# Optimization experiments

Hardware: AMD Instinct MI355X
Metric: run time of the kernel (lower is better)

The kernel has to match this reference:

```python
import jax, jax.numpy as jnp
import numpy as np

D = 256      # d_model
H = 8        # n_heads
L = 6        # n_layers
F = 1024     # ffn_hidden
MAXB = 50    # max_boids
S = MAXB + 3 # seq len: CLS + ctx + predator + boids
B = 4096
VH = 256     # value_hidden_dim
DH = D // H


def setup_inputs() -> dict:
    key = jax.random.key(0)
    ks = jax.random.split(key, 20)
    r = lambda i, shape: jax.random.normal(ks[i], shape, jnp.float32) * 0.02
    return {
        "observation": jax.random.normal(ks[0], (B, 4 + 4 * MAXB), jnp.float32),
        "cls_emb": r(1, (D,)), "type_cls": r(2, (D,)), "type_ctx": r(3, (D,)),
        "type_pred": r(4, (D,)), "type_boid": r(5, (D,)),
        "ctx_W": r(6, (2, D)), "ctx_b": jnp.zeros((D,), jnp.float32),
        "pred_W": r(7, (4, D)), "pred_b": jnp.zeros((D,), jnp.float32),
        "boid_W": r(8, (4, D)), "boid_b": jnp.zeros((D,), jnp.float32),
        "qkv_W": r(9, (L, D, 3 * D)), "qkv_b": jnp.zeros((L, 3 * D), jnp.float32),
        "out_W": r(10, (L, D, D)), "out_b": jnp.zeros((L, D), jnp.float32),
        "ln1_g": jnp.ones((L, D), jnp.float32), "ln1_b": jnp.zeros((L, D), jnp.float32),
        "ffn_W1": r(11, (L, D, F)), "ffn_b1": jnp.zeros((L, F), jnp.float32),
        "ffn_W2": r(12, (L, F, D)), "ffn_b2": jnp.zeros((L, D), jnp.float32),
        "ln2_g": jnp.ones((L, D), jnp.float32), "ln2_b": jnp.zeros((L, D), jnp.float32),
        "proj_W": r(13, (D, 2)), "proj_b": jnp.zeros((2,), jnp.float32),
        "vh_W1": r(14, (D, VH)), "vh_b1": jnp.zeros((VH,), jnp.float32),
        "vh_W2": r(15, (VH, VH)), "vh_b2": jnp.zeros((VH,), jnp.float32),
        "vh_W3": r(16, (VH, 1)), "vh_b3": jnp.zeros((1,), jnp.float32),
    }


def _ln(x, g, b):
    m = jnp.mean(x, axis=-1, keepdims=True)
    v = jnp.mean((x - m) ** 2, axis=-1, keepdims=True)
    return (x - m) * jax.lax.rsqrt(v + 1e-5) * g + b


def reference(observation, cls_emb, type_cls, type_ctx, type_pred, type_boid,
              ctx_W, ctx_b, pred_W, pred_b, boid_W, boid_b,
              qkv_W, qkv_b, out_W, out_b, ln1_g, ln1_b,
              ffn_W1, ffn_b1, ffn_W2, ffn_b2, ln2_g, ln2_b,
              proj_W, proj_b, vh_W1, vh_b1, vh_W2, vh_b2, vh_W3, vh_b3):
    Bn = observation.shape[0]
    ctx = observation[:, :2]                                   # [B,2]
    pred = jnp.concatenate([observation[:, 2:4],
                            jnp.zeros_like(observation[:, :2])], axis=-1)  # [B,4]
    boids = observation[:, 4:].reshape(Bn, MAXB, 4)            # [B,MAXB,4]

    # All-zero boid slots are skipped; valid boids are packed to the front
    # (stable order preserved), then zero-padded -- vectorized via stable argsort.
    valid = jnp.any(boids != 0, axis=-1)                       # [B,MAXB]
    order = jnp.argsort(~valid, axis=1, stable=True)           # valid first
    packed = jnp.take_along_axis(boids, order[:, :, None], axis=1)
    vs = jnp.take_along_axis(valid, order, axis=1)             # [B,MAXB]

    cls_tok = jnp.broadcast_to(cls_emb + type_cls, (Bn, 1, D))
    ctx_tok = (ctx @ ctx_W + ctx_b + type_ctx)[:, None, :]
    pred_tok = (pred @ pred_W + pred_b + type_pred)[:, None, :]
    boid_tok = (packed @ boid_W + boid_b + type_boid) * vs[:, :, None]  # pad -> zeros
    x = jnp.concatenate([cls_tok, ctx_tok, pred_tok, boid_tok], axis=1)  # [B,S,D]

    pad = jnp.concatenate([jnp.zeros((Bn, 3), bool), ~vs], axis=1)       # [B,S]
    neg = jnp.where(pad, -1e9, 0.0)[:, None, None, :]                    # [B,1,1,S]

    scale = 1.0 / np.sqrt(DH)
    for i in range(L):  # post-LN encoder layers (ReLU FFN)
        qkv = x @ qkv_W[i] + qkv_b[i]                                    # [B,S,3D]
        q, k, v = jnp.split(qkv, 3, axis=-1)
        q = q.reshape(Bn, S, H, DH).transpose(0, 2, 1, 3)
        k = k.reshape(Bn, S, H, DH).transpose(0, 2, 1, 3)
        v = v.reshape(Bn, S, H, DH).transpose(0, 2, 1, 3)
        scores = jnp.einsum('bhqd,bhkd->bhqk', q, k) * scale + neg
        a = jax.nn.softmax(scores, axis=-1)
        o = jnp.einsum('bhqk,bhkd->bhqd', a, v).transpose(0, 2, 1, 3).reshape(Bn, S, D)
        x = _ln(x + o @ out_W[i] + out_b[i], ln1_g[i], ln1_b[i])
        h = jax.nn.relu(x @ ffn_W1[i] + ffn_b1[i])
        x = _ln(x + h @ ffn_W2[i] + ffn_b2[i], ln2_g[i], ln2_b[i])

    cls_f = x[:, 0]                                                      # [B,D]
    action_mean = jnp.tanh(cls_f @ proj_W + proj_b)                      # [B,2]
    h = jax.nn.relu(cls_f @ vh_W1 + vh_b1)
    h = jax.nn.relu(h @ vh_W2 + vh_b2)
    value = h @ vh_W3 + vh_b3                                            # [B,1]
    return jnp.concatenate([action_mean, value], axis=-1)                # [B,3]
```

## Files before the change

### kernel.cpp

```cpp
#include <hip/hip_runtime.h>
#include <hip/hip_bf16.h>
#include <stdint.h>

typedef unsigned short u16;
typedef short s16x8 __attribute__((ext_vector_type(8)));
typedef float f32x4 __attribute__((ext_vector_type(4)));

#define D_ 256
#define H_ 8
#define L_ 6
#define F_ 1024
#define MAXB_ 50
#define S_ 53
#define B_ 4096

__device__ __forceinline__ u16 f2b(float f){
  __hip_bfloat16 h = __float2bfloat16(f);
  return *reinterpret_cast<u16*>(&h);
}
__device__ __forceinline__ float b2f(u16 u){
  __hip_bfloat16 h = *reinterpret_cast<__hip_bfloat16*>(&u);
  return __bfloat162float(h);
}

__device__ __forceinline__ void gload16(const void* g, void* l){
  __builtin_amdgcn_global_load_lds((__attribute__((address_space(1))) void*)(g),
                                   (__attribute__((address_space(3))) void*)(l), 16, 0, 0);
}

__global__ __launch_bounds__(256) void prep_weights(
    const float* __restrict__ qkvW, const float* __restrict__ outW,
    const float* __restrict__ w1,   const float* __restrict__ w2,
    u16* __restrict__ qkvT, u16* __restrict__ outT,
    u16* __restrict__ w1T,  u16* __restrict__ w2T)
{
  const int i = blockIdx.x * 256 + threadIdx.x;
  if (i < L_*768*256) {
    const int l = i / (768*256); const int r = i % (768*256);
    const int n = r >> 8; const int k = r & 255;
    qkvT[i] = f2b(qkvW[((size_t)l*256 + k)*768 + n]);
  }
  if (i < L_*256*256) {
    const int l = i >> 16; const int r = i & 65535;
    const int n = r >> 8; const int k = r & 255;
    outT[i] = f2b(outW[((size_t)l*256 + k)*256 + n]);
  }
  if (i < L_*1024*256) {
    const int l = i / (1024*256); const int r = i % (1024*256);
    const int n = r >> 8; const int k = r & 255;
    w1T[i] = f2b(w1[((size_t)l*256 + k)*1024 + n]);
  }
  if (i < L_*256*1024) {
    const int l = i / (256*1024); const int r = i % (256*1024);
    const int n = r >> 10; const int k = r & 1023;
    w2T[i] = f2b(w2[((size_t)l*1024 + k)*256 + n]);
  }
}

__global__ __launch_bounds__(256) void embed_kernel(
    const float* __restrict__ obs,
    const float* __restrict__ cls_emb, const float* __restrict__ type_cls,
    const float* __restrict__ type_ctx, const float* __restrict__ type_pred,
    const float* __restrict__ type_boid,
    const float* __restrict__ ctxW, const float* __restrict__ ctxb,
    const float* __restrict__ predW, const float* __restrict__ predb,
    const float* __restrict__ boidW, const float* __restrict__ boidb,
    u16* __restrict__ xbf, int* __restrict__ nvalid)
{
  const int b = blockIdx.x, tid = threadIdx.x;
  __shared__ float obs_s[204];
  __shared__ int perm_s[MAXB_];
  __shared__ int count_s;
  const float* orow = obs + (size_t)b * 204;
  if (tid < 204) obs_s[tid] = orow[tid];
  __syncthreads();
  if (tid < 64) {
    const int j = tid;
    bool flag = false;
    if (j < MAXB_) {
      const float a0=obs_s[4+4*j], a1=obs_s[5+4*j], a2=obs_s[6+4*j], a3=obs_s[7+4*j];
      flag = (a0!=0.f)||(a1!=0.f)||(a2!=0.f)||(a3!=0.f);
    }
    const unsigned long long m = __ballot(flag);
    if (flag) perm_s[__popcll(m & ((1ull<<j)-1ull))] = j;
    if (j == 0) { count_s = __popcll(m); nvalid[b] = __popcll(m); }
  }
  __syncthreads();
  const int cnt = count_s;
  const int d = tid;
  for (int s = 0; s < S_; ++s) {
    float v;
    if (s == 0)      v = cls_emb[d] + type_cls[d];
    else if (s == 1) v = obs_s[0]*ctxW[d] + obs_s[1]*ctxW[256+d] + ctxb[d] + type_ctx[d];
    else if (s == 2) v = obs_s[2]*predW[d] + obs_s[3]*predW[256+d] + predb[d] + type_pred[d];
    else {
      const int j = s - 3;
      if (j < cnt) {
        const int bj = perm_s[j];
        v = obs_s[4+4*bj]*boidW[d] + obs_s[5+4*bj]*boidW[256+d]
          + obs_s[6+4*bj]*boidW[512+d] + obs_s[7+4*bj]*boidW[768+d]
          + boidb[d] + type_boid[d];
      } else v = 0.f;
    }
    xbf[((size_t)b*S_ + s)*256 + d] = f2b(v);
  }
}

template<bool RELU>
__global__ __launch_bounds__(256, 2) void gemm_bias_kernel(
    const u16* __restrict__ A, const u16* __restrict__ Bt,
    const float* __restrict__ bias, u16* __restrict__ C,
    int N, int K)
{
  __shared__ __attribute__((aligned(16))) u16 As[128*64];
  __shared__ __attribute__((aligned(16))) u16 Bs[128*64];
  const int tid = threadIdx.x;
  const int w = tid >> 6, lane = tid & 63;
  const int wr = w >> 1, wc = w & 1;
  const int lm = lane & 15, lg = lane >> 4;
  const int lrow = lane >> 3, lcol = (lane & 7) * 8;
  const int m0 = blockIdx.x * 128, n0 = blockIdx.y * 128;

  f32x4 acc[4][4];
  #pragma unroll
  for (int m=0;m<4;m++)
    #pragma unroll
    for (int n=0;n<4;n++)
      #pragma unroll
      for (int t=0;t<4;t++) acc[m][n][t] = 0.f;

  for (int k0 = 0; k0 < K; k0 += 64) {
    #pragma unroll
    for (int j=0;j<4;j++){
      const int chunk = w*4 + j;
      const int row = chunk*8 + lrow;
      gload16(A  + (size_t)(m0+row)*K + k0 + lcol, &As[chunk*512]);
      gload16(Bt + (size_t)(n0+row)*K + k0 + lcol, &Bs[chunk*512]);
    }
    __syncthreads();
    #pragma unroll
    for (int kk=0;kk<64;kk+=32){
      s16x8 af[4], bfr[4];
      #pragma unroll
      for (int m=0;m<4;m++) af[m] = *reinterpret_cast<const s16x8*>(&As[(wr*64 + m*16 + lm)*64 + kk + lg*8]);
      #pragma unroll
      for (int n=0;n<4;n++) bfr[n] = *reinterpret_cast<const s16x8*>(&Bs[(wc*64 + n*16 + lm)*64 + kk + lg*8]);
      #pragma unroll
      for (int m=0;m<4;m++)
        #pragma unroll
        for (int n=0;n<4;n++)
          acc[m][n] = __builtin_amdgcn_mfma_f32_16x16x32_bf16(af[m], bfr[n], acc[m][n], 0, 0, 0);
    }
    __syncthreads();
  }

  #pragma unroll
  for (int n=0;n<4;n++){
    const int col = n0 + wc*64 + n*16 + lm;
    const float bv = bias[col];
    #pragma unroll
    for (int m=0;m<4;m++){
      const int r0 = m0 + wr*64 + m*16 + lg*4;
      #pragma unroll
      for (int j=0;j<4;j++){
        float v = acc[m][n][j] + bv;
        if (RELU) v = fmaxf(v, 0.f);
        C[(size_t)(r0+j)*N + col] = f2b(v);
      }
    }
  }
}

__global__ __launch_bounds__(64) void attn_kernel(
    const u16* __restrict__ qkv, u16* __restrict__ O, const int* __restrict__ nvalid)
{
  const int bh = blockIdx.x;
  const int b = bh >> 3, h = bh & 7;
  const int lane = threadIdx.x;
  const int lm = lane & 15, lg = lane >> 4;
  __shared__ __attribute__((aligned(16))) u16 Pl[64*72];
  __shared__ __attribute__((aligned(16))) u16 VT[32*72];
  const size_t base = (size_t)b * S_ * 768;

  s16x8 aQ[4], aK[4];
  #pragma unroll
  for (int t=0;t<4;t++){
    const int r = t*16 + lm;
    if (r < S_){
      aQ[t] = *reinterpret_cast<const s16x8*>(&qkv[base + (size_t)r*768 +       h*32 + lg*8]);
      aK[t] = *reinterpret_cast<const s16x8*>(&qkv[base + (size_t)r*768 + 256 + h*32 + lg*8]);
    } else {
      #pragma unroll
      for (int i=0;i<8;i++){ aQ[t][i]=0; aK[t][i]=0; }
    }
  }
  {
    const int s = lane;
    #pragma unroll
    for (int i4=0;i4<4;i4++){
      s16x8 v;
      if (s < S_) v = *reinterpret_cast<const s16x8*>(&qkv[base + (size_t)s*768 + 512 + h*32 + i4*8]);
      else {
        #pragma unroll
        for (int i=0;i<8;i++) v[i]=0;
      }
      #pragma unroll
      for (int t=0;t<8;t++) VT[(i4*8+t)*72 + s] = (u16)v[t];
    }
  }
  f32x4 zf;
  #pragma unroll
  for (int t=0;t<4;t++) zf[t] = 0.f;
  f32x4 sc[4][4];
  #pragma unroll
  for (int qi=0;qi<4;qi++)
    #pragma unroll
    for (int kj=0;kj<4;kj++)
      sc[qi][kj] = __builtin_amdgcn_mfma_f32_16x16x32_bf16(aQ[qi], aK[kj], zf, 0, 0, 0);

  const int T = 3 + nvalid[b];
  const float scale = 0.17677669529663689f;
  __syncthreads();

  #pragma unroll
  for (int qi=0;qi<4;qi++){
    #pragma unroll
    for (int j=0;j<4;j++){
      float v[4];
      #pragma unroll
      for (int kj=0;kj<4;kj++)
        v[kj] = sc[qi][kj][j]*scale + ((kj*16+lm) < T ? 0.f : -1e9f);
      float mx = fmaxf(fmaxf(v[0],v[1]), fmaxf(v[2],v[3]));
      mx = fmaxf(mx, __shfl_xor(mx, 1));
      mx = fmaxf(mx, __shfl_xor(mx, 2));
      mx = fmaxf(mx, __shfl_xor(mx, 4));
      mx = fmaxf(mx, __shfl_xor(mx, 8));
      float e[4]; float sum = 0.f;
      #pragma unroll
      for (int kj=0;kj<4;kj++){ e[kj] = __expf(v[kj]-mx); sum += e[kj]; }
      sum += __shfl_xor(sum, 1);
      sum += __shfl_xor(sum, 2);
      sum += __shfl_xor(sum, 4);
      sum += __shfl_xor(sum, 8);
      const float inv = 1.f / sum;
      const int q = qi*16 + lg*4 + j;
      #pragma unroll
      for (int kj=0;kj<4;kj++) Pl[q*72 + kj*16 + lm] = f2b(e[kj]*inv);
    }
  }
  __syncthreads();

  s16x8 bV[2][2];
  #pragma unroll
  for (int c=0;c<2;c++)
    #pragma unroll
    for (int dj=0;dj<2;dj++)
      bV[c][dj] = *reinterpret_cast<const s16x8*>(&VT[(dj*16+lm)*72 + c*32 + lg*8]);

  f32x4 oa[4][2];
  #pragma unroll
  for (int qi=0;qi<4;qi++)
    #pragma unroll
    for (int dj=0;dj<2;dj++)
      #pragma unroll
      for (int t=0;t<4;t++) oa[qi][dj][t] = 0.f;

  #pragma unroll
  for (int qi=0;qi<4;qi++){
    #pragma unroll
    for (int c=0;c<2;c++){
      const s16x8 aP = *reinterpret_cast<const s16x8*>(&Pl[(qi*16+lm)*72 + c*32 + lg*8]);
      #pragma unroll
      for (int dj=0;dj<2;dj++)
        oa[qi][dj] = __builtin_amdgcn_mfma_f32_16x16x32_bf16(aP, bV[c][dj], oa[qi][dj], 0, 0, 0);
    }
  }
  #pragma unroll
  for (int qi=0;qi<4;qi++)
    #pragma unroll
    for (int dj=0;dj<2;dj++)
      #pragma unroll
      for (int j=0;j<4;j++){
        const int q = qi*16 + lg*4 + j;
        if (q < S_)
          O[((size_t)(b*S_ + q))*256 + h*32 + dj*16 + lm] = f2b(oa[qi][dj][j]);
      }
}

__global__ __launch_bounds__(256, 2) void gemm_ln_kernel(
    const u16* __restrict__ A, const u16* __restrict__ Bt,
    const float* __restrict__ bias, const float* __restrict__ lng, const float* __restrict__ lnb,
    u16* __restrict__ xbf, int K)
{
  __shared__ __attribute__((aligned(16))) u16 As[64*64];
  __shared__ __attribute__((aligned(16))) u16 Bs[256*64];
  __shared__ float redS[4][64];
  __shared__ float redQ[4][64];
  const int tid = threadIdx.x;
  const int w = tid >> 6, lane = tid & 63;
  const int lm = lane & 15, lg = lane >> 4;
  const int lrow = lane >> 3, lcol = (lane & 7)*8;
  const int m0 = blockIdx.x * 64;

  f32x4 acc[4][4];
  #pragma unroll
  for (int m=0;m<4;m++)
    #pragma unroll
    for (int n=0;n<4;n++)
      #pragma unroll
      for (int t=0;t<4;t++) acc[m][n][t] = 0.f;

  for (int k0 = 0; k0 < K; k0 += 64) {
    #pragma unroll
    for (int j=0;j<2;j++){
      const int chunk = w*2 + j;
      const int row = chunk*8 + lrow;
      gload16(A + (size_t)(m0+row)*K + k0 + lcol, &As[chunk*512]);
    }
    #pragma unroll
    for (int j=0;j<8;j++){
      const int chunk = w*8 + j;
      const int row = chunk*8 + lrow;
      gload16(Bt + (size_t)row*K + k0 + lcol, &Bs[chunk*512]);
    }
    __syncthreads();
    #pragma unroll
    for (int kk=0;kk<64;kk+=32){
      s16x8 af[4], bfr[4];
      #pragma unroll
      for (int m=0;m<4;m++) af[m] = *reinterpret_cast<const s16x8*>(&As[(m*16 + lm)*64 + kk + lg*8]);
      #pragma unroll
      for (int n=0;n<4;n++) bfr[n] = *reinterpret_cast<const s16x8*>(&Bs[(w*64 + n*16 + lm)*64 + kk + lg*8]);
      #pragma unroll
      for (int m=0;m<4;m++)
        #pragma unroll
        for (int n=0;n<4;n++)
          acc[m][n] = __builtin_amdgcn_mfma_f32_16x16x32_bf16(af[m], bfr[n], acc[m][n], 0, 0, 0);
    }
    __syncthreads();
  }

  float bb[4];
  #pragma unroll
  for (int n=0;n<4;n++) bb[n] = bias[w*64 + n*16 + lm];
  #pragma unroll
  for (int m=0;m<4;m++)
    #pragma unroll
    for (int j=0;j<4;j++){
      const int r = m*16 + lg*4 + j;
      const u16* resp = xbf + (size_t)(m0+r)*256 + w*64 + lm;
      #pragma unroll
      for (int n=0;n<4;n++) acc[m][n][j] += bb[n] + b2f(resp[n*16]);
    }

  #pragma unroll
  for (int m=0;m<4;m++)
    #pragma unroll
    for (int j=0;j<4;j++){
      float s1 = 0.f, s2 = 0.f;
      #pragma unroll
      for (int n=0;n<4;n++){ const float t = acc[m][n][j]; s1 += t; s2 += t*t; }
      s1 += __shfl_xor(s1, 1); s2 += __shfl_xor(s2, 1);
      s1 += __shfl_xor(s1, 2); s2 += __shfl_xor(s2, 2);
      s1 += __shfl_xor(s1, 4); s2 += __shfl_xor(s2, 4);
      s1 += __shfl_xor(s1, 8); s2 += __shfl_xor(s2, 8);
      if (lm == 0){ const int r = m*16 + lg*4 + j; redS[w][r] = s1; redQ[w][r] = s2; }
    }
  __syncthreads();

  float gg[4], be[4];
  #pragma unroll
  for (int n=0;n<4;n++){ const int col = w*64 + n*16 + lm; gg[n] = lng[col]; be[n] = lnb[col]; }
  #pragma unroll
  for (int m=0;m<4;m++)
    #pragma unroll
    for (int j=0;j<4;j++){
      const int r = m*16 + lg*4 + j;
      const float sum = redS[0][r]+redS[1][r]+redS[2][r]+redS[3][r];
      const float sq  = redQ[0][r]+redQ[1][r]+redQ[2][r]+redQ[3][r];
      const float mean = sum * (1.f/256.f);
      const float var  = sq  * (1.f/256.f) - mean*mean;
      const float rstd = rsqrtf(var + 1e-5f);
      #pragma unroll
      for (int n=0;n<4;n++){
        const float y = (acc[m][n][j] - mean)*rstd*gg[n] + be[n];
        xbf[(size_t)(m0+r)*256 + w*64 + n*16 + lm] = f2b(y);
      }
    }
}

__global__ __launch_bounds__(256) void head_kernel(
    const u16* __restrict__ xbf,
    const float* __restrict__ projW, const float* __restrict__ projb,
    const float* __restrict__ W1, const float* __restrict__ b1,
    const float* __restrict__ W2, const float* __restrict__ b2,
    const float* __restrict__ W3, const float* __restrict__ b3,
    float* __restrict__ out)
{
  const int b = blockIdx.x, tid = threadIdx.x;
  __shared__ float c_s[256];
  __shared__ float h_s[256];
  __shared__ float red[3][4];
  const float c = b2f(xbf[((size_t)b*S_)*256 + tid]);
  c_s[tid] = c;
  __syncthreads();
  float a1 = b1[tid];
  #pragma unroll 8
  for (int k=0;k<256;k++) a1 += c_s[k]*W1[k*256+tid];
  a1 = fmaxf(a1, 0.f);
  h_s[tid] = a1;
  __syncthreads();
  float a2 = b2[tid];
  #pragma unroll 8
  for (int k=0;k<256;k++) a2 += h_s[k]*W2[k*256+tid];
  a2 = fmaxf(a2, 0.f);

  float pv = a2 * W3[tid];
  float p0 = c * projW[tid*2];
  float p1 = c * projW[tid*2+1];
  #pragma unroll
  for (int o=1;o<64;o<<=1){
    pv += __shfl_xor(pv, o);
    p0 += __shfl_xor(p0, o);
    p1 += __shfl_xor(p1, o);
  }
  const int w = tid >> 6;
  if ((tid & 63) == 0){ red[0][w]=p0; red[1][w]=p1; red[2][w]=pv; }
  __syncthreads();
  if (tid == 0){
    const float q0 = red[0][0]+red[0][1]+red[0][2]+red[0][3] + projb[0];
    const float q1 = red[1][0]+red[1][1]+red[1][2]+red[1][3] + projb[1];
    const float qv = red[2][0]+red[2][1]+red[2][2]+red[2][3] + b3[0];
    out[b*3+0] = tanhf(q0);
    out[b*3+1] = tanhf(q1);
    out[b*3+2] = qv;
  }
}

__global__ void fallback_ws(float* out, int n, float val){
  const int i = blockIdx.x*256 + threadIdx.x;
  if (i < n) out[i] = val;
}

extern "C" void kernel_launch(void* const* d_in, const int* in_sizes, int n_in,
                              void* d_out, int out_size, void* d_ws, size_t ws_size,
                              hipStream_t stream)
{
  (void)in_sizes; (void)n_in;
  const float* obs      = (const float*)d_in[0];
  const float* cls_emb  = (const float*)d_in[1];
  const float* type_cls = (const float*)d_in[2];
  const float* type_ctx = (const float*)d_in[3];
  const float* type_pred= (const float*)d_in[4];
  const float* type_boid= (const float*)d_in[5];
  const float* ctx_W    = (const float*)d_in[6];
  const float* ctx_b    = (const float*)d_in[7];
  const float* pred_W   = (const float*)d_in[8];
  const float* pred_b   = (const float*)d_in[9];
  const float* boid_W   = (const float*)d_in[10];
  const float* boid_b   = (const float*)d_in[11];
  const float* qkv_W    = (const float*)d_in[12];
  const float* qkv_b    = (const float*)d_in[13];
  const float* out_W    = (const float*)d_in[14];
  const float* out_b    = (const float*)d_in[15];
  const float* ln1_g    = (const float*)d_in[16];
  const float* ln1_b    = (const float*)d_in[17];
  const float* ffn_W1   = (const float*)d_in[18];
  const float* ffn_b1   = (const float*)d_in[19];
  const float* ffn_W2   = (const float*)d_in[20];
  const float* ffn_b2   = (const float*)d_in[21];
  const float* ln2_g    = (const float*)d_in[22];
  const float* ln2_b    = (const float*)d_in[23];
  const float* proj_W   = (const float*)d_in[24];
  const float* proj_b   = (const float*)d_in[25];
  const float* vh_W1    = (const float*)d_in[26];
  const float* vh_b1    = (const float*)d_in[27];
  const float* vh_W2    = (const float*)d_in[28];
  const float* vh_b2    = (const float*)d_in[29];
  const float* vh_W3    = (const float*)d_in[30];
  const float* vh_b3    = (const float*)d_in[31];

  const size_t SZ_WQ = (size_t)L_*768*256*2;
  const size_t SZ_WO = (size_t)L_*256*256*2;
  const size_t SZ_W1 = (size_t)L_*1024*256*2;
  const size_t SZ_W2 = (size_t)L_*256*1024*2;
  const size_t SZ_W  = SZ_WQ + SZ_WO + SZ_W1 + SZ_W2;

  int Bc = 0;
  const int cand[6] = {4096, 2048, 1024, 512, 256, 128};
  for (int i = 0; i < 6; ++i) {
    const size_t need = SZ_W + (size_t)cand[i]*162816ull + (size_t)cand[i]*4ull + 4096ull;
    if (need <= ws_size) { Bc = cand[i]; break; }
  }
  if (Bc == 0) {
    const float val = 2000.0f + (float)(ws_size >> 20);
    fallback_ws<<<(out_size+255)/256, 256, 0, stream>>>((float*)d_out, out_size, val);
    return;
  }
  const int NC = B_ / Bc;
  const size_t Mc = (size_t)Bc * S_;

  char* ws = (char*)d_ws;
  u16* wq  = (u16*)(ws);
  u16* wo  = (u16*)(ws + SZ_WQ);
  u16* w1t = (u16*)(ws + SZ_WQ + SZ_WO);
  u16* w2t = (u16*)(ws + SZ_WQ + SZ_WO + SZ_W1);
  char* act = ws + SZ_W;
  u16* xbf  = (u16*)(act);
  u16* big  = (u16*)(act + Mc*512);
  u16* obuf = (u16*)(act + Mc*512 + Mc*2048);
  int* nval = (int*)(act + Mc*512 + Mc*2048 + Mc*512);

  prep_weights<<<6144, 256, 0, stream>>>(qkv_W, out_W, ffn_W1, ffn_W2, wq, wo, w1t, w2t);

  for (int c = 0; c < NC; ++c) {
    const size_t b0 = (size_t)c * Bc;
    embed_kernel<<<Bc, 256, 0, stream>>>(obs + b0*204,
        cls_emb, type_cls, type_ctx, type_pred, type_boid,
        ctx_W, ctx_b, pred_W, pred_b, boid_W, boid_b,
        xbf, nval);
    for (int l = 0; l < L_; ++l) {
      gemm_bias_kernel<false><<<dim3((int)(Mc/128), 6), 256, 0, stream>>>(
          xbf, wq + (size_t)l*768*256, qkv_b + l*768, big, 768, 256);
      attn_kernel<<<Bc*H_, 64, 0, stream>>>(big, obuf, nval);
      gemm_ln_kernel<<<(int)(Mc/64), 256, 0, stream>>>(
          obuf, wo + (size_t)l*256*256, out_b + l*256, ln1_g + l*256, ln1_b + l*256,
          xbf, 256);
      gemm_bias_kernel<true><<<dim3((int)(Mc/128), 8), 256, 0, stream>>>(
          xbf, w1t + (size_t)l*1024*256, ffn_b1 + l*1024, big, 1024, 256);
      gemm_ln_kernel<<<(int)(Mc/64), 256, 0, stream>>>(
          big, w2t + (size_t)l*256*1024, ffn_b2 + l*256, ln2_g + l*256, ln2_b + l*256,
          xbf, 1024);
    }
    head_kernel<<<Bc, 256, 0, stream>>>(xbf, proj_W, proj_b, vh_W1, vh_b1, vh_W2, vh_b2,
                                        vh_W3, vh_b3, (float*)d_out + b0*3);
  }
}
```

Before: 5.792 ms.

## Replace tiled GEMM with weight-stationary register GEMM, swizzle LDS in LN GEMM

The QKV and FFN1 GEMMs become a weight-stationary persistent kernel. Each wave keeps a 32-column slice of the weight matrix in registers for the full K=256 and loops over 16-row strips of A read straight from global memory, with no LDS staging. The gemm_ln kernel gets an XOR swizzle on its LDS layout to cut bank conflicts. The batch chunk size is now derived from the available workspace in multiples of 64 instead of powers of two, so more of the batch fits in one chunk. The risks are that A is re-read from global without LDS reuse and that the weight slice raises register pressure.

```diff
diff --git a/kernel.cpp b/kernel.cpp
--- a/kernel.cpp
+++ b/kernel.cpp
@@ -106,68 +106,50 @@
   }
 }
 
-template<bool RELU>
-__global__ __launch_bounds__(256, 2) void gemm_bias_kernel(
+template<int N, bool RELU>
+__global__ __launch_bounds__(256, 3) void wsgemm_kernel(
     const u16* __restrict__ A, const u16* __restrict__ Bt,
-    const float* __restrict__ bias, u16* __restrict__ C,
-    int N, int K)
-{
-  __shared__ __attribute__((aligned(16))) u16 As[128*64];
-  __shared__ __attribute__((aligned(16))) u16 Bs[128*64];
+    const float* __restrict__ bias, u16* __restrict__ C, int M)
+{
   const int tid = threadIdx.x;
   const int w = tid >> 6, lane = tid & 63;
-  const int wr = w >> 1, wc = w & 1;
   const int lm = lane & 15, lg = lane >> 4;
-  const int lrow = lane >> 3, lcol = (lane & 7) * 8;
-  const int m0 = blockIdx.x * 128, n0 = blockIdx.y * 128;
-
-  f32x4 acc[4][4];
-  #pragma unroll
-  for (int m=0;m<4;m++)
-    #pragma unroll
-    for (int n=0;n<4;n++)
-      #pragma unroll
-      for (int t=0;t<4;t++) acc[m][n][t] = 0.f;
-
-  for (int k0 = 0; k0 < K; k0 += 64) {
-    #pragma unroll
-    for (int j=0;j<4;j++){
-      const int chunk = w*4 + j;
-      const int row = chunk*8 + lrow;
-      gload16(A  + (size_t)(m0+row)*K + k0 + lcol, &As[chunk*512]);
-      gload16(Bt + (size_t)(n0+row)*K + k0 + lcol, &Bs[chunk*512]);
-    }
-    __syncthreads();
-    #pragma unroll
-    for (int kk=0;kk<64;kk+=32){
-      s16x8 af[4], bfr[4];
-      #pragma unroll
-      for (int m=0;m<4;m++) af[m] = *reinterpret_cast<const s16x8*>(&As[(wr*64 + m*16 + lm)*64 + kk + lg*8]);
-      #pragma unroll
-      for (int n=0;n<4;n++) bfr[n] = *reinterpret_cast<const s16x8*>(&Bs[(wc*64 + n*16 + lm)*64 + kk + lg*8]);
-      #pragma unroll
-      for (int m=0;m<4;m++)
-        #pragma unroll
-        for (int n=0;n<4;n++)
-          acc[m][n] = __builtin_amdgcn_mfma_f32_16x16x32_bf16(af[m], bfr[n], acc[m][n], 0, 0, 0);
-    }
-    __syncthreads();
-  }
-
-  #pragma unroll
-  for (int n=0;n<4;n++){
-    const int col = n0 + wc*64 + n*16 + lm;
-    const float bv = bias[col];
-    #pragma unroll
-    for (int m=0;m<4;m++){
-      const int r0 = m0 + wr*64 + m*16 + lg*4;
+  const int ncol0 = blockIdx.y * 128 + w * 32;
+
+  s16x8 bfr[2][8];
+  float bv[2];
+  #pragma unroll
+  for (int n=0;n<2;n++){
+    bv[n] = bias[ncol0 + n*16 + lm];
+    #pragma unroll
+    for (int k=0;k<8;k++)
+      bfr[n][k] = *reinterpret_cast<const s16x8*>(&Bt[(size_t)(ncol0+n*16+lm)*256 + k*32 + lg*8]);
+  }
+
+  const int step = gridDim.x << 4;
+  for (int r0 = blockIdx.x*16; r0 < M; r0 += step) {
+    s16x8 afr[8];
+    #pragma unroll
+    for (int k=0;k<8;k++)
+      afr[k] = *reinterpret_cast<const s16x8*>(&A[(size_t)(r0+lm)*256 + k*32 + lg*8]);
+    f32x4 acc[2];
+    #pragma unroll
+    for (int n=0;n<2;n++)
+      #pragma unroll
+      for (int t=0;t<4;t++) acc[n][t] = 0.f;
+    #pragma unroll
+    for (int k=0;k<8;k++)
+      #pragma unroll
+      for (int n=0;n<2;n++)
+        acc[n] = __builtin_amdgcn_mfma_f32_16x16x32_bf16(afr[k], bfr[n][k], acc[n], 0, 0, 0);
+    #pragma unroll
+    for (int n=0;n<2;n++)
       #pragma unroll
       for (int j=0;j<4;j++){
-        float v = acc[m][n][j] + bv;
+        float v = acc[n][j] + bv[n];
         if (RELU) v = fmaxf(v, 0.f);
-        C[(size_t)(r0+j)*N + col] = f2b(v);
+        C[(size_t)(r0+lg*4+j)*N + ncol0 + n*16 + lm] = f2b(v);
       }
-    }
   }
 }
 
@@ -299,8 +281,11 @@
   const int tid = threadIdx.x;
   const int w = tid >> 6, lane = tid & 63;
   const int lm = lane & 15, lg = lane >> 4;
-  const int lrow = lane >> 3, lcol = (lane & 7)*8;
+  const int lrow = lane >> 3;
+  const int lxor = ((lane & 7) ^ lrow) * 8;
   const int m0 = blockIdx.x * 64;
+  const int cb0 = ((lg*16) ^ ((lm & 7) << 4));
+  const int cb1 = ((64 + lg*16) ^ ((lm & 7) << 4));
 
   f32x4 acc[4][4];
   #pragma unroll
@@ -309,28 +294,30 @@
     for (int n=0;n<4;n++)
       #pragma unroll
       for (int t=0;t<4;t++) acc[m][n][t] = 0.f;
+
+  const char* Ab = (const char*)As;
+  const char* Bb = (const char*)Bs;
 
   for (int k0 = 0; k0 < K; k0 += 64) {
     #pragma unroll
     for (int j=0;j<2;j++){
       const int chunk = w*2 + j;
-      const int row = chunk*8 + lrow;
-      gload16(A + (size_t)(m0+row)*K + k0 + lcol, &As[chunk*512]);
+      gload16(A + (size_t)(m0 + chunk*8 + lrow)*K + k0 + lxor, &As[chunk*512]);
     }
     #pragma unroll
     for (int j=0;j<8;j++){
       const int chunk = w*8 + j;
-      const int row = chunk*8 + lrow;
-      gload16(Bt + (size_t)row*K + k0 + lcol, &Bs[chunk*512]);
+      gload16(Bt + (size_t)(chunk*8 + lrow)*K + k0 + lxor, &Bs[chunk*512]);
     }
     __syncthreads();
     #pragma unroll
-    for (int kk=0;kk<64;kk+=32){
+    for (int kk=0;kk<2;kk++){
+      const int cb = kk ? cb1 : cb0;
       s16x8 af[4], bfr[4];
       #pragma unroll
-      for (int m=0;m<4;m++) af[m] = *reinterpret_cast<const s16x8*>(&As[(m*16 + lm)*64 + kk + lg*8]);
-      #pragma unroll
-      for (int n=0;n<4;n++) bfr[n] = *reinterpret_cast<const s16x8*>(&Bs[(w*64 + n*16 + lm)*64 + kk + lg*8]);
+      for (int m=0;m<4;m++) af[m]  = *reinterpret_cast<const s16x8*>(Ab + (m*16 + lm)*128 + cb);
+      #pragma unroll
+      for (int n=0;n<4;n++) bfr[n] = *reinterpret_cast<const s16x8*>(Bb + (w*64 + n*16 + lm)*128 + cb);
       #pragma unroll
       for (int m=0;m<4;m++)
         #pragma unroll
@@ -486,19 +473,16 @@
   const size_t SZ_W2 = (size_t)L_*256*1024*2;
   const size_t SZ_W  = SZ_WQ + SZ_WO + SZ_W1 + SZ_W2;
 
-  int Bc = 0;
-  const int cand[6] = {4096, 2048, 1024, 512, 256, 128};
-  for (int i = 0; i < 6; ++i) {
-    const size_t need = SZ_W + (size_t)cand[i]*162816ull + (size_t)cand[i]*4ull + 4096ull;
-    if (need <= ws_size) { Bc = cand[i]; break; }
-  }
-  if (Bc == 0) {
+  size_t avail = (ws_size > SZ_W + 8192) ? (ws_size - SZ_W - 8192) : 0;
+  long long bcm = (long long)(avail / 135684ull);
+  if (bcm > B_) bcm = B_;
+  int Bc_max = (int)((bcm / 64) * 64);
+  if (Bc_max < 64) {
     const float val = 2000.0f + (float)(ws_size >> 20);
     fallback_ws<<<(out_size+255)/256, 256, 0, stream>>>((float*)d_out, out_size, val);
     return;
   }
-  const int NC = B_ / Bc;
-  const size_t Mc = (size_t)Bc * S_;
+  const size_t Mc_max = (size_t)Bc_max * S_;
 
   char* ws = (char*)d_ws;
   u16* wq  = (u16*)(ws);
@@ -507,32 +491,35 @@
   u16* w2t = (u16*)(ws + SZ_WQ + SZ_WO + SZ_W1);
   char* act = ws + SZ_W;
   u16* xbf  = (u16*)(act);
-  u16* big  = (u16*)(act + Mc*512);
-  u16* obuf = (u16*)(act + Mc*512 + Mc*2048);
-  int* nval = (int*)(act + Mc*512 + Mc*2048 + Mc*512);
+  u16* big  = (u16*)(act + Mc_max*512);
+  u16* obuf = big + Mc_max*768;
+  int* nval = (int*)(act + Mc_max*512 + Mc_max*2048);
 
   prep_weights<<<6144, 256, 0, stream>>>(qkv_W, out_W, ffn_W1, ffn_W2, wq, wo, w1t, w2t);
 
-  for (int c = 0; c < NC; ++c) {
-    const size_t b0 = (size_t)c * Bc;
-    embed_kernel<<<Bc, 256, 0, stream>>>(obs + b0*204,
+  int b0 = 0;
+  while (b0 < B_) {
+    const int Bc = (B_ - b0 < Bc_max) ? (B_ - b0) : Bc_max;
+    const int Mc = Bc * S_;
+    embed_kernel<<<Bc, 256, 0, stream>>>(obs + (size_t)b0*204,
         cls_emb, type_cls, type_ctx, type_pred, type_boid,
         ctx_W, ctx_b, pred_W, pred_b, boid_W, boid_b,
         xbf, nval);
     for (int l = 0; l < L_; ++l) {
-      gemm_bias_kernel<false><<<dim3((int)(Mc/128), 6), 256, 0, stream>>>(
-          xbf, wq + (size_t)l*768*256, qkv_b + l*768, big, 768, 256);
+      wsgemm_kernel<768,false><<<dim3(128, 6), 256, 0, stream>>>(
+          xbf, wq + (size_t)l*768*256, qkv_b + l*768, big, Mc);
       attn_kernel<<<Bc*H_, 64, 0, stream>>>(big, obuf, nval);
-      gemm_ln_kernel<<<(int)(Mc/64), 256, 0, stream>>>(
+      gemm_ln_kernel<<<Mc/64, 256, 0, stream>>>(
           obuf, wo + (size_t)l*256*256, out_b + l*256, ln1_g + l*256, ln1_b + l*256,
           xbf, 256);
-      gemm_bias_kernel<true><<<dim3((int)(Mc/128), 8), 256, 0, stream>>>(
-          xbf, w1t + (size_t)l*1024*256, ffn_b1 + l*1024, big, 1024, 256);
-      gemm_ln_kernel<<<(int)(Mc/64), 256, 0, stream>>>(
+      wsgemm_kernel<1024,true><<<dim3(96, 8), 256, 0, stream>>>(
+          xbf, w1t + (size_t)l*1024*256, ffn_b1 + l*1024, big, Mc);
+      gemm_ln_kernel<<<Mc/64, 256, 0, stream>>>(
           big, w2t + (size_t)l*256*1024, ffn_b2 + l*256, ln2_g + l*256, ln2_b + l*256,
           xbf, 1024);
     }
     head_kernel<<<Bc, 256, 0, stream>>>(xbf, proj_W, proj_b, vh_W1, vh_b1, vh_W2, vh_b2,
-                                        vh_W3, vh_b3, (float*)d_out + b0*3);
-  }
-}
+                                        vh_W3, vh_b3, (float*)d_out + (size_t)b0*3);
+    b0 += Bc;
+  }
+}
```

New measurement: 7.799 ms. 34.6% more time.

## Double-buffer and swizzle GEMM LDS tiles, widen LN GEMM tile, enlarge batch chunks

Applied to the files above, without the earlier changes.

Both GEMM kernels now use double-buffered LDS tiles, so the next K-tile is fetched while MFMAs run on the current one. An XOR swizzle on the LDS column layout is meant to cut bank conflicts on fragment reads. The GEMM+LayerNorm kernel moves to 128-row tiles with 512 threads (8 waves in a 2x4 layout), which halves how often the shared weight tile is reloaded per row. The attention output buffer now reuses the unused tail of the big activation buffer, and the batch chunk size is derived from the workspace, allowing larger chunks and fewer launches. The cost is more LDS per block, which may lower occupancy.

```diff
diff --git a/kernel.cpp b/kernel.cpp
--- a/kernel.cpp
+++ b/kernel.cpp
@@ -112,14 +112,17 @@
     const float* __restrict__ bias, u16* __restrict__ C,
     int N, int K)
 {
-  __shared__ __attribute__((aligned(16))) u16 As[128*64];
-  __shared__ __attribute__((aligned(16))) u16 Bs[128*64];
+  __shared__ __attribute__((aligned(16))) u16 As[2][128*64];
+  __shared__ __attribute__((aligned(16))) u16 Bs[2][128*64];
   const int tid = threadIdx.x;
   const int w = tid >> 6, lane = tid & 63;
   const int wr = w >> 1, wc = w & 1;
   const int lm = lane & 15, lg = lane >> 4;
-  const int lrow = lane >> 3, lcol = (lane & 7) * 8;
+  const int lrow = lane >> 3;
+  const int lxor = ((lane & 7) ^ lrow) * 8;
   const int m0 = blockIdx.x * 128, n0 = blockIdx.y * 128;
+  const int cb0 = (lg*16) ^ ((lm & 7) << 4);
+  const int cb1 = (64 + lg*16) ^ ((lm & 7) << 4);
 
   f32x4 acc[4][4];
   #pragma unroll
@@ -129,22 +132,38 @@
       #pragma unroll
       for (int t=0;t<4;t++) acc[m][n][t] = 0.f;
 
-  for (int k0 = 0; k0 < K; k0 += 64) {
-    #pragma unroll
-    for (int j=0;j<4;j++){
-      const int chunk = w*4 + j;
-      const int row = chunk*8 + lrow;
-      gload16(A  + (size_t)(m0+row)*K + k0 + lcol, &As[chunk*512]);
-      gload16(Bt + (size_t)(n0+row)*K + k0 + lcol, &Bs[chunk*512]);
-    }
-    __syncthreads();
-    #pragma unroll
-    for (int kk=0;kk<64;kk+=32){
+  #pragma unroll
+  for (int j=0;j<4;j++){
+    const int chunk = w*4 + j;
+    const int row = chunk*8 + lrow;
+    gload16(A  + (size_t)(m0+row)*K + lxor, &As[0][chunk*512]);
+    gload16(Bt + (size_t)(n0+row)*K + lxor, &Bs[0][chunk*512]);
+  }
+  __syncthreads();
+
+  const int NT = K >> 6;
+  for (int t = 0; t < NT; ++t) {
+    const int cur = t & 1;
+    if (t + 1 < NT) {
+      const int k0 = (t+1) << 6;
+      #pragma unroll
+      for (int j=0;j<4;j++){
+        const int chunk = w*4 + j;
+        const int row = chunk*8 + lrow;
+        gload16(A  + (size_t)(m0+row)*K + k0 + lxor, &As[cur^1][chunk*512]);
+        gload16(Bt + (size_t)(n0+row)*K + k0 + lxor, &Bs[cur^1][chunk*512]);
+      }
+    }
+    const char* Ab = (const char*)As[cur];
+    const char* Bb = (const char*)Bs[cur];
+    #pragma unroll
+    for (int kk=0;kk<2;kk++){
+      const int cb = kk ? cb1 : cb0;
       s16x8 af[4], bfr[4];
       #pragma unroll
-      for (int m=0;m<4;m++) af[m] = *reinterpret_cast<const s16x8*>(&As[(wr*64 + m*16 + lm)*64 + kk + lg*8]);
-      #pragma unroll
-      for (int n=0;n<4;n++) bfr[n] = *reinterpret_cast<const s16x8*>(&Bs[(wc*64 + n*16 + lm)*64 + kk + lg*8]);
+      for (int m=0;m<4;m++) af[m]  = *reinterpret_cast<const s16x8*>(Ab + (wr*64 + m*16 + lm)*128 + cb);
+      #pragma unroll
+      for (int n=0;n<4;n++) bfr[n] = *reinterpret_cast<const s16x8*>(Bb + (wc*64 + n*16 + lm)*128 + cb);
       #pragma unroll
       for (int m=0;m<4;m++)
         #pragma unroll
@@ -287,20 +306,24 @@
       }
 }
 
-__global__ __launch_bounds__(256, 2) void gemm_ln_kernel(
+__global__ __launch_bounds__(512, 2) void gemm_ln_kernel(
     const u16* __restrict__ A, const u16* __restrict__ Bt,
     const float* __restrict__ bias, const float* __restrict__ lng, const float* __restrict__ lnb,
     u16* __restrict__ xbf, int K)
 {
-  __shared__ __attribute__((aligned(16))) u16 As[64*64];
-  __shared__ __attribute__((aligned(16))) u16 Bs[256*64];
-  __shared__ float redS[4][64];
-  __shared__ float redQ[4][64];
+  __shared__ __attribute__((aligned(16))) u16 As[2][128*64];
+  __shared__ __attribute__((aligned(16))) u16 Bs[2][256*64];
+  __shared__ float redS[4][128];
+  __shared__ float redQ[4][128];
   const int tid = threadIdx.x;
   const int w = tid >> 6, lane = tid & 63;
+  const int wr = w >> 2, wc = w & 3;
   const int lm = lane & 15, lg = lane >> 4;
-  const int lrow = lane >> 3, lcol = (lane & 7)*8;
-  const int m0 = blockIdx.x * 64;
+  const int lrow = lane >> 3;
+  const int lxor = ((lane & 7) ^ lrow) * 8;
+  const int m0 = blockIdx.x * 128;
+  const int cb0 = (lg*16) ^ ((lm & 7) << 4);
+  const int cb1 = (64 + lg*16) ^ ((lm & 7) << 4);
 
   f32x4 acc[4][4];
   #pragma unroll
@@ -310,27 +333,44 @@
       #pragma unroll
       for (int t=0;t<4;t++) acc[m][n][t] = 0.f;
 
-  for (int k0 = 0; k0 < K; k0 += 64) {
-    #pragma unroll
-    for (int j=0;j<2;j++){
-      const int chunk = w*2 + j;
-      const int row = chunk*8 + lrow;
-      gload16(A + (size_t)(m0+row)*K + k0 + lcol, &As[chunk*512]);
-    }
-    #pragma unroll
-    for (int j=0;j<8;j++){
-      const int chunk = w*8 + j;
-      const int row = chunk*8 + lrow;
-      gload16(Bt + (size_t)row*K + k0 + lcol, &Bs[chunk*512]);
-    }
-    __syncthreads();
-    #pragma unroll
-    for (int kk=0;kk<64;kk+=32){
+  #pragma unroll
+  for (int j=0;j<2;j++){
+    const int chunk = w*2 + j;
+    gload16(A + (size_t)(m0 + chunk*8 + lrow)*K + lxor, &As[0][chunk*512]);
+  }
+  #pragma unroll
+  for (int j=0;j<4;j++){
+    const int chunk = w*4 + j;
+    gload16(Bt + (size_t)(chunk*8 + lrow)*K + lxor, &Bs[0][chunk*512]);
+  }
+  __syncthreads();
+
+  const int NT = K >> 6;
+  for (int t = 0; t < NT; ++t) {
+    const int cur = t & 1;
+    if (t + 1 < NT) {
+      const int k0 = (t+1) << 6;
+      #pragma unroll
+      for (int j=0;j<2;j++){
+        const int chunk = w*2 + j;
+        gload16(A + (size_t)(m0 + chunk*8 + lrow)*K + k0 + lxor, &As[cur^1][chunk*512]);
+      }
+      #pragma unroll
+      for (int j=0;j<4;j++){
+        const int chunk = w*4 + j;
+        gload16(Bt + (size_t)(chunk*8 + lrow)*K + k0 + lxor, &Bs[cur^1][chunk*512]);
+      }
+    }
+    const char* Ab = (const char*)As[cur];
+    const char* Bb = (const char*)Bs[cur];
+    #pragma unroll
+    for (int kk=0;kk<2;kk++){
+      const int cb = kk ? cb1 : cb0;
       s16x8 af[4], bfr[4];
       #pragma unroll
-      for (int m=0;m<4;m++) af[m] = *reinterpret_cast<const s16x8*>(&As[(m*16 + lm)*64 + kk + lg*8]);
-      #pragma unroll
-      for (int n=0;n<4;n++) bfr[n] = *reinterpret_cast<const s16x8*>(&Bs[(w*64 + n*16 + lm)*64 + kk + lg*8]);
+      for (int m=0;m<4;m++) af[m]  = *reinterpret_cast<const s16x8*>(Ab + (wr*64 + m*16 + lm)*128 + cb);
+      #pragma unroll
+      for (int n=0;n<4;n++) bfr[n] = *reinterpret_cast<const s16x8*>(Bb + (wc*64 + n*16 + lm)*128 + cb);
       #pragma unroll
       for (int m=0;m<4;m++)
         #pragma unroll
@@ -342,13 +382,13 @@
 
   float bb[4];
   #pragma unroll
-  for (int n=0;n<4;n++) bb[n] = bias[w*64 + n*16 + lm];
+  for (int n=0;n<4;n++) bb[n] = bias[wc*64 + n*16 + lm];
   #pragma unroll
   for (int m=0;m<4;m++)
     #pragma unroll
     for (int j=0;j<4;j++){
-      const int r = m*16 + lg*4 + j;
-      const u16* resp = xbf + (size_t)(m0+r)*256 + w*64 + lm;
+      const int r = wr*64 + m*16 + lg*4 + j;
+      const u16* resp = xbf + (size_t)(m0+r)*256 + wc*64 + lm;
       #pragma unroll
       for (int n=0;n<4;n++) acc[m][n][j] += bb[n] + b2f(resp[n*16]);
     }
@@ -359,23 +399,23 @@
     for (int j=0;j<4;j++){
       float s1 = 0.f, s2 = 0.f;
       #pragma unroll
-      for (int n=0;n<4;n++){ const float t = acc[m][n][j]; s1 += t; s2 += t*t; }
+      for (int n=0;n<4;n++){ const float t2 = acc[m][n][j]; s1 += t2; s2 += t2*t2; }
       s1 += __shfl_xor(s1, 1); s2 += __shfl_xor(s2, 1);
       s1 += __shfl_xor(s1, 2); s2 += __shfl_xor(s2, 2);
       s1 += __shfl_xor(s1, 4); s2 += __shfl_xor(s2, 4);
       s1 += __shfl_xor(s1, 8); s2 += __shfl_xor(s2, 8);
-      if (lm == 0){ const int r = m*16 + lg*4 + j; redS[w][r] = s1; redQ[w][r] = s2; }
+      if (lm == 0){ const int r = wr*64 + m*16 + lg*4 + j; redS[wc][r] = s1; redQ[wc][r] = s2; }
     }
   __syncthreads();
 
   float gg[4], be[4];
   #pragma unroll
-  for (int n=0;n<4;n++){ const int col = w*64 + n*16 + lm; gg[n] = lng[col]; be[n] = lnb[col]; }
+  for (int n=0;n<4;n++){ const int col = wc*64 + n*16 + lm; gg[n] = lng[col]; be[n] = lnb[col]; }
   #pragma unroll
   for (int m=0;m<4;m++)
     #pragma unroll
     for (int j=0;j<4;j++){
-      const int r = m*16 + lg*4 + j;
+      const int r = wr*64 + m*16 + lg*4 + j;
       const float sum = redS[0][r]+redS[1][r]+redS[2][r]+redS[3][r];
       const float sq  = redQ[0][r]+redQ[1][r]+redQ[2][r]+redQ[3][r];
       const float mean = sum * (1.f/256.f);
@@ -384,7 +424,7 @@
       #pragma unroll
       for (int n=0;n<4;n++){
         const float y = (acc[m][n][j] - mean)*rstd*gg[n] + be[n];
-        xbf[(size_t)(m0+r)*256 + w*64 + n*16 + lm] = f2b(y);
+        xbf[(size_t)(m0+r)*256 + wc*64 + n*16 + lm] = f2b(y);
       }
     }
 }
@@ -486,19 +526,16 @@
   const size_t SZ_W2 = (size_t)L_*256*1024*2;
   const size_t SZ_W  = SZ_WQ + SZ_WO + SZ_W1 + SZ_W2;
 
-  int Bc = 0;
-  const int cand[6] = {4096, 2048, 1024, 512, 256, 128};
-  for (int i = 0; i < 6; ++i) {
-    const size_t need = SZ_W + (size_t)cand[i]*162816ull + (size_t)cand[i]*4ull + 4096ull;
-    if (need <= ws_size) { Bc = cand[i]; break; }
-  }
-  if (Bc == 0) {
+  size_t avail = (ws_size > SZ_W + 8192) ? (ws_size - SZ_W - 8192) : 0;
+  long long bcm = (long long)(avail / 135684ull);
+  if (bcm > B_) bcm = B_;
+  int Bc_max = (int)((bcm / 128) * 128);
+  if (Bc_max < 128) {
     const float val = 2000.0f + (float)(ws_size >> 20);
     fallback_ws<<<(out_size+255)/256, 256, 0, stream>>>((float*)d_out, out_size, val);
     return;
   }
-  const int NC = B_ / Bc;
-  const size_t Mc = (size_t)Bc * S_;
+  const size_t Mc_max = (size_t)Bc_max * S_;
 
   char* ws = (char*)d_ws;
   u16* wq  = (u16*)(ws);
@@ -507,32 +544,35 @@
   u16* w2t = (u16*)(ws + SZ_WQ + SZ_WO + SZ_W1);
   char* act = ws + SZ_W;
   u16* xbf  = (u16*)(act);
-  u16* big  = (u16*)(act + Mc*512);
-  u16* obuf = (u16*)(act + Mc*512 + Mc*2048);
-  int* nval = (int*)(act + Mc*512 + Mc*2048 + Mc*512);
+  u16* big  = (u16*)(act + Mc_max*512);
+  u16* obuf = big + Mc_max*768;
+  int* nval = (int*)(act + Mc_max*512 + Mc_max*2048);
 
   prep_weights<<<6144, 256, 0, stream>>>(qkv_W, out_W, ffn_W1, ffn_W2, wq, wo, w1t, w2t);
 
-  for (int c = 0; c < NC; ++c) {
-    const size_t b0 = (size_t)c * Bc;
-    embed_kernel<<<Bc, 256, 0, stream>>>(obs + b0*204,
+  int b0 = 0;
+  while (b0 < B_) {
+    const int Bc = (B_ - b0 < Bc_max) ? (B_ - b0) : Bc_max;
+    const int Mc = Bc * S_;
+    embed_kernel<<<Bc, 256, 0, stream>>>(obs + (size_t)b0*204,
         cls_emb, type_cls, type_ctx, type_pred, type_boid,
         ctx_W, ctx_b, pred_W, pred_b, boid_W, boid_b,
         xbf, nval);
     for (int l = 0; l < L_; ++l) {
-      gemm_bias_kernel<false><<<dim3((int)(Mc/128), 6), 256, 0, stream>>>(
+      gemm_bias_kernel<false><<<dim3(Mc/128, 6), 256, 0, stream>>>(
           xbf, wq + (size_t)l*768*256, qkv_b + l*768, big, 768, 256);
       attn_kernel<<<Bc*H_, 64, 0, stream>>>(big, obuf, nval);
-      gemm_ln_kernel<<<(int)(Mc/64), 256, 0, stream>>>(
+      gemm_ln_kernel<<<Mc/128, 512, 0, stream>>>(
           obuf, wo + (size_t)l*256*256, out_b + l*256, ln1_g + l*256, ln1_b + l*256,
           xbf, 256);
-      gemm_bias_kernel<true><<<dim3((int)(Mc/128), 8), 256, 0, stream>>>(
+      gemm_bias_kernel<true><<<dim3(Mc/128, 8), 256, 0, stream>>>(
           xbf, w1t + (size_t)l*1024*256, ffn_b1 + l*1024, big, 1024, 256);
-      gemm_ln_kernel<<<(int)(Mc/64), 256, 0, stream>>>(
+      gemm_ln_kernel<<<Mc/128, 512, 0, stream>>>(
           big, w2t + (size_t)l*256*1024, ffn_b2 + l*256, ln2_g + l*256, ln2_b + l*256,
           xbf, 1024);
     }
     head_kernel<<<Bc, 256, 0, stream>>>(xbf, proj_W, proj_b, vh_W1, vh_b1, vh_W2, vh_b2,
-                                        vh_W3, vh_b3, (float*)d_out + b0*3);
-  }
-}
+                                        vh_W3, vh_b3, (float*)d_out + (size_t)b0*3);
+    b0 += Bc;
+  }
+}
```

New measurement: 5.532 ms. 1.05x faster.
